# Optimization experiments

Hardware: AMD Instinct MI355X
Metric: run time of the kernel (lower is better)

Reference implementation:

```python
import jax, jax.numpy as jnp
import numpy as np

EPS = 1e-6
NEG_SLOPE = 0.2
B, C, E, F = 8, 2048, 256, 256


def setup_inputs() -> dict:
    key = jax.random.key(0)
    k1, k2, k3, k4, k5, k6 = jax.random.split(key, 6)
    X = jax.random.normal(k1, (B, C, E, 3), dtype=jnp.float32)
    J = jax.random.normal(k2, (B, C, E, 3), dtype=jnp.float32)
    A = jax.random.normal(k3, (F, E), dtype=jnp.float32)
    Bw = jax.random.normal(k4, (F, E), dtype=jnp.float32)
    Cw = jax.random.normal(k5, (F, E), dtype=jnp.float32)
    # VNLeakyReLU map_to_dir weight [F, F] (nn.Linear-style scale)
    W = jax.random.normal(k6, (F, F), dtype=jnp.float32) / jnp.sqrt(jnp.float32(F))
    return {"X": X, "J": J, "A": A, "Bw": Bw, "Cw": Cw, "W": W}


def _basis(J):
    # normalized direction [B,C,E,3]
    nJ = J / (jnp.linalg.norm(J, axis=-1, keepdims=True) + EPS)
    sub = nJ[..., :2]                                   # [B,C,E,2]
    Uz = -(sub * sub).sum(-1) / (nJ[..., 2] + EPS)      # [B,C,E]
    U = jnp.concatenate([sub, Uz[..., None]], axis=-1)  # [B,C,E,3]
    nU = U / (jnp.linalg.norm(U, axis=-1, keepdims=True) + EPS)
    nV = jnp.cross(nU, nJ)                              # [B,C,E,3]
    # rows of R are (U, V, J): R[..., i, j] matches torch reshape of cat
    return jnp.stack([nU, nV, nJ], axis=-2)             # [B,C,E,3,3]


def reference(X, J, A, Bw, Cw, W):
    R = _basis(J)                                        # [B,C,E,3,3]
    RT = jnp.swapaxes(R, -1, -2)                         # [B,C,E,3,3]
    # rtx[..., i] = RT[..., i, :] . X  (per torch get_rtx)
    rtx = jnp.einsum('bceij,bcej->bcei', RT, X)          # [B,C,E,3]

    def rrtx(i, r):
        # indexed_R = R[..., :, i]; broadcast-multiply by scalar field r
        return R[..., :, i] * r[..., None]               # [B,C,E,3]

    a = rrtx(0, rtx[..., 0]) + rrtx(1, rtx[..., 1])
    b = rrtx(1, rtx[..., 0]) - rrtx(0, rtx[..., 1])
    c = rrtx(2, rtx[..., 2])
    Y = (jnp.einsum('fe,bcei->bcfi', A, a)
         + jnp.einsum('fe,bcei->bcfi', Bw, b)
         + jnp.einsum('fe,bcei->bcfi', Cw, c))           # [B,C,F,3]

    x = jnp.transpose(Y, (0, 2, 3, 1))                   # [B,F,3,C]
    # VNLeakyReLU: direction d via linear over feature dim
    d = jnp.einsum('fg,bgic->bfic', W, x)                # [B,F,3,C]
    dot = (x * d).sum(axis=2, keepdims=True)             # [B,F,1,C]
    mask = (dot >= 0).astype(x.dtype)
    dns = (d * d).sum(axis=2, keepdims=True)
    x_out = (NEG_SLOPE * x
             + (1.0 - NEG_SLOPE) * (mask * x
                                    + (1.0 - mask) * (x - dot / (dns + EPS) * d)))
    return x_out
```

## Files before the change

### kernel.cpp

```cpp
#include <hip/hip_runtime.h>


constexpr float EPSf  = 1e-6f;
constexpr int Bdim = 8, Cdim = 2048, Edim = 256, Fdim = 256;
constexpr int NT  = 16;
constexpr int KC1 = 24;
constexpr int KC2 = 8;
constexpr int ZLD = 776;
constexpr int YLD = 264;
constexpr int M_ROWS = KC1 * 16 * 64;
constexpr int W_ROWS = KC2 * 16 * 64;

typedef __attribute__((ext_vector_type(8))) _Float16 half8;
typedef __attribute__((ext_vector_type(4))) _Float16 half4;
typedef __attribute__((ext_vector_type(4))) float    f32x4;

__device__ __forceinline__ void basis_abc(float Xx, float Xy, float Xz,
                                          float Jx, float Jy, float Jz,
                                          float* a, float* bb, float* cc)
{
    const float jn  = sqrtf(Jx*Jx + Jy*Jy + Jz*Jz) + EPSf;
    const float rj  = __builtin_amdgcn_rcpf(jn);
    const float nJz = Jz * rj;
    const float h   = (Jx*Jx + Jy*Jy) * (rj * rj);
    const float Uz  = -h * __builtin_amdgcn_rcpf(nJz + EPSf);
    const float un  = sqrtf(h + Uz*Uz) + EPSf;
    const float mx  = Uz * __builtin_amdgcn_rcpf(un);
    const float mz  = nJz;
    const float t   = mx*Xx + mz*Xz;
    a[0]  = Xx - mx*t;   a[1]  = Xy;            a[2]  = Xz - mz*t;
    bb[0] = mz*Xy;       bb[1] = mx*Xz - mz*Xx; bb[2] = -(mx*Xy);
    cc[0] = mx*t;        cc[1] = 0.f;           cc[2] = mz*t;
}

__global__ __launch_bounds__(256)
void prep_weights_f16(const float* __restrict__ Ap, const float* __restrict__ Bp,
                      const float* __restrict__ Cp, const float* __restrict__ Wp,
                      _Float16* __restrict__ ws)
{
    const int tid = blockIdx.x * 256 + threadIdx.x;
    const bool isW = tid >= M_ROWS;
    const int row = isW ? tid - M_ROWS : tid;
    const int l   = row & 63;
    const int ft  = (row >> 6) & 15;
    const int kc  = row >> 10;
    const int f   = ft * 16 + (l & 15);
    const int k0  = kc * 32 + ((l >> 4) << 3);

    const float* src;
    int e0;
    if (isW)            { src = Wp; e0 = k0; }
    else if (k0 < 256)  { src = Ap; e0 = k0; }
    else if (k0 < 512)  { src = Bp; e0 = k0 - 256; }
    else                { src = Cp; e0 = k0 - 512; }

    const float* p = src + f * 256 + e0;
    half8 v;
    #pragma unroll
    for (int j = 0; j < 8; ++j) v[j] = (_Float16)p[j];

    _Float16* dst = ws + (isW ? (size_t)M_ROWS * 8 : 0);
    *reinterpret_cast<half8*>(dst + (size_t)row * 8) = v;
}

__global__ __launch_bounds__(512, 4)
void fused_mfma_f16(const float* __restrict__ Xp, const float* __restrict__ Jp,
                    const _Float16* __restrict__ wsM, const _Float16* __restrict__ wsW,
                    float* __restrict__ outp)
{
    __shared__ __align__(16) _Float16 lds[48 * ZLD];

    const int t  = threadIdx.x;
    const int s0 = blockIdx.x * NT;
    const int b  = s0 >> 11;
    const int c0 = s0 & (Cdim - 1);

    {
        const int equad = t & 63;
        const int sq    = t >> 6;
        const int e0    = equad * 4;
        #pragma unroll
        for (int ss = 0; ss < 2; ++ss) {
            const int s = sq * 2 + ss;
            const long site = (long)(b * Cdim + c0 + s);
            const float4* X4 = reinterpret_cast<const float4*>(Xp) + site * 192 + equad * 3;
            const float4* J4 = reinterpret_cast<const float4*>(Jp) + site * 192 + equad * 3;
            const float4 xA = X4[0], xB = X4[1], xC = X4[2];
            const float4 jA = J4[0], jB = J4[1], jC = J4[2];
            const float xf[12] = {xA.x,xA.y,xA.z,xA.w, xB.x,xB.y,xB.z,xB.w, xC.x,xC.y,xC.z,xC.w};
            const float jf[12] = {jA.x,jA.y,jA.z,jA.w, jB.x,jB.y,jB.z,jB.w, jC.x,jC.y,jC.z,jC.w};

            half4 za[3], zb[3], zc[3];
            #pragma unroll
            for (int ee = 0; ee < 4; ++ee) {
                float a[3], bb[3], cc[3];
                basis_abc(xf[3*ee], xf[3*ee+1], xf[3*ee+2],
                          jf[3*ee], jf[3*ee+1], jf[3*ee+2], a, bb, cc);
                #pragma unroll
                for (int i = 0; i < 3; ++i) {
                    za[i][ee] = (_Float16)a[i];
                    zb[i][ee] = (_Float16)bb[i];
                    zc[i][ee] = (_Float16)cc[i];
                }
            }
            #pragma unroll
            for (int i = 0; i < 3; ++i) {
                _Float16* rowp = &lds[(i * NT + s) * ZLD];
                *reinterpret_cast<half4*>(rowp +       e0) = za[i];
                *reinterpret_cast<half4*>(rowp + 256 + e0) = zb[i];
                *reinterpret_cast<half4*>(rowp + 512 + e0) = zc[i];
            }
        }
    }
    __syncthreads();

    const int wid = t >> 6;
    const int l   = t & 63;
    const int lr  = l & 15;
    const int lk  = (l >> 4) * 8;

    f32x4 Yacc[2][3];
    #pragma unroll
    for (int q = 0; q < 2; ++q)
        #pragma unroll
        for (int nt = 0; nt < 3; ++nt)
            Yacc[q][nt] = f32x4{0.f, 0.f, 0.f, 0.f};

    const half8* Mf = reinterpret_cast<const half8*>(wsM);
    for (int kc = 0; kc < KC1; ++kc) {
        half8 af[2];
        #pragma unroll
        for (int q = 0; q < 2; ++q)
            af[q] = Mf[(kc * 16 + wid * 2 + q) * 64 + l];
        half8 zf[3];
        #pragma unroll
        for (int nt = 0; nt < 3; ++nt)
            zf[nt] = *reinterpret_cast<const half8*>(&lds[(nt * NT + lr) * ZLD + kc * 32 + lk]);
        #pragma unroll
        for (int q = 0; q < 2; ++q)
            #pragma unroll
            for (int nt = 0; nt < 3; ++nt)
                Yacc[q][nt] = __builtin_amdgcn_mfma_f32_16x16x32_f16(af[q], zf[nt], Yacc[q][nt], 0, 0, 0);
    }
    __syncthreads();

    #pragma unroll
    for (int q = 0; q < 2; ++q) {
        const int row = (wid * 2 + q) * 16 + (l >> 4) * 4;
        #pragma unroll
        for (int nt = 0; nt < 3; ++nt) {
            const int col = nt * NT + lr;
            half4 v = { (_Float16)Yacc[q][nt][0], (_Float16)Yacc[q][nt][1],
                        (_Float16)Yacc[q][nt][2], (_Float16)Yacc[q][nt][3] };
            *reinterpret_cast<half4*>(&lds[col * YLD + row]) = v;
        }
    }
    __syncthreads();

    f32x4 Dacc[2][3];
    #pragma unroll
    for (int q = 0; q < 2; ++q)
        #pragma unroll
        for (int nt = 0; nt < 3; ++nt)
            Dacc[q][nt] = f32x4{0.f, 0.f, 0.f, 0.f};

    const half8* Wf = reinterpret_cast<const half8*>(wsW);
    for (int kc = 0; kc < KC2; ++kc) {
        half8 af[2];
        #pragma unroll
        for (int q = 0; q < 2; ++q)
            af[q] = Wf[(kc * 16 + wid * 2 + q) * 64 + l];
        half8 yf[3];
        #pragma unroll
        for (int nt = 0; nt < 3; ++nt)
            yf[nt] = *reinterpret_cast<const half8*>(&lds[(nt * NT + lr) * YLD + kc * 32 + lk]);
        #pragma unroll
        for (int q = 0; q < 2; ++q)
            #pragma unroll
            for (int nt = 0; nt < 3; ++nt)
                Dacc[q][nt] = __builtin_amdgcn_mfma_f32_16x16x32_f16(af[q], yf[nt], Dacc[q][nt], 0, 0, 0);
    }

    #pragma unroll
    for (int q = 0; q < 2; ++q) {
        const int fbase = (wid * 2 + q) * 16 + (l >> 4) * 4;
        #pragma unroll
        for (int r = 0; r < 4; ++r) {
#pragma clang fp contract(off)
            const float x0 = Yacc[q][0][r], x1 = Yacc[q][1][r], x2 = Yacc[q][2][r];
            const float d0 = Dacc[q][0][r], d1 = Dacc[q][1][r], d2 = Dacc[q][2][r];
            const float dot = (x0*d0 + x1*d1) + x2*d2;
            const float dns = (d0*d0 + d1*d1) + d2*d2;
            const float sc  = dot / (dns + EPSf);
            const bool  pos = (dot >= 0.f);
            const int f = fbase + r;
            const long obase = ((long)(b * Fdim + f) * 3) * Cdim + c0 + lr;
            const float c0v = pos ? x0 : (x0 - sc*d0);
            const float c1v = pos ? x1 : (x1 - sc*d1);
            const float c2v = pos ? x2 : (x2 - sc*d2);
            outp[obase + 0 * Cdim] = 0.2f*x0 + 0.8f*c0v;
            outp[obase + 1 * Cdim] = 0.2f*x1 + 0.8f*c1v;
            outp[obase + 2 * Cdim] = 0.2f*x2 + 0.8f*c2v;
        }
    }
}

__device__ __forceinline__ float comp(const float4& v, int k) {
    return k == 0 ? v.x : k == 1 ? v.y : k == 2 ? v.z : v.w;
}

__global__ __launch_bounds__(256)
void fused_cl_lrelu_fp32(const float* __restrict__ Xp, const float* __restrict__ Jp,
                         const float* __restrict__ Ap, const float* __restrict__ Bp,
                         const float* __restrict__ Cp, const float* __restrict__ Wp,
                         float* __restrict__ outp)
{
    __shared__ float4 sabc[4 * Edim * 3];
    __shared__ float  ylds[4 * 3][Fdim];

    const int t   = threadIdx.x;
    const int s0  = blockIdx.x * 4;
    const int b   = s0 / Cdim;
    const int c0  = s0 % Cdim;

    #pragma unroll
    for (int r = 0; r < 4; ++r) {
        const int e  = t;
        const int idx = ((b * Cdim + c0 + r) * Edim + e) * 3;
        float a[3], bb[3], cc[3];
        basis_abc(Xp[idx], Xp[idx+1], Xp[idx+2], Jp[idx], Jp[idx+1], Jp[idx+2], a, bb, cc);
        const int base = (r * Edim + e) * 3;
        sabc[base + 0] = make_float4(a[0], a[1], a[2], bb[0]);
        sabc[base + 1] = make_float4(bb[1], bb[2], cc[0], cc[1]);
        sabc[base + 2] = make_float4(cc[2], 0.f, 0.f, 0.f);
    }
    __syncthreads();

    const int fl = t & 63;
    const int cg = t >> 6;
    float Y[4][3];
    #pragma unroll
    for (int q = 0; q < 4; ++q) Y[q][0] = Y[q][1] = Y[q][2] = 0.f;

    const float4* A4 = reinterpret_cast<const float4*>(Ap);
    const float4* B4 = reinterpret_cast<const float4*>(Bp);
    const float4* C4 = reinterpret_cast<const float4*>(Cp);
    for (int e4 = 0; e4 < Edim / 4; ++e4) {
        float4 wa[4], wb[4], wc[4];
        #pragma unroll
        for (int q = 0; q < 4; ++q) {
            const int f = q * 64 + fl;
            wa[q] = A4[f * (Edim/4) + e4];
            wb[q] = B4[f * (Edim/4) + e4];
            wc[q] = C4[f * (Edim/4) + e4];
        }
        #pragma unroll
        for (int k = 0; k < 4; ++k) {
            const int e = e4 * 4 + k;
            const float4 p0 = sabc[(cg * Edim + e) * 3 + 0];
            const float4 p1 = sabc[(cg * Edim + e) * 3 + 1];
            const float4 p2 = sabc[(cg * Edim + e) * 3 + 2];
            #pragma unroll
            for (int q = 0; q < 4; ++q) {
                const float Af = comp(wa[q], k), Bf = comp(wb[q], k), Cf = comp(wc[q], k);
                Y[q][0] += Af * p0.x + Bf * p0.w + Cf * p1.z;
                Y[q][1] += Af * p0.y + Bf * p1.x + Cf * p1.w;
                Y[q][2] += Af * p0.z + Bf * p1.y + Cf * p2.x;
            }
        }
    }
    #pragma unroll
    for (int q = 0; q < 4; ++q) {
        const int f = q * 64 + fl;
        ylds[cg * 3 + 0][f] = Y[q][0];
        ylds[cg * 3 + 1][f] = Y[q][1];
        ylds[cg * 3 + 2][f] = Y[q][2];
    }
    __syncthreads();

    float D[4][3];
    #pragma unroll
    for (int q = 0; q < 4; ++q) D[q][0] = D[q][1] = D[q][2] = 0.f;
    const float4* W4 = reinterpret_cast<const float4*>(Wp);
    for (int g4 = 0; g4 < Fdim / 4; ++g4) {
        float4 ww[4];
        #pragma unroll
        for (int q = 0; q < 4; ++q) ww[q] = W4[(q * 64 + fl) * (Fdim/4) + g4];
        const float4 y0 = *reinterpret_cast<const float4*>(&ylds[cg * 3 + 0][g4 * 4]);
        const float4 y1 = *reinterpret_cast<const float4*>(&ylds[cg * 3 + 1][g4 * 4]);
        const float4 y2 = *reinterpret_cast<const float4*>(&ylds[cg * 3 + 2][g4 * 4]);
        #pragma unroll
        for (int k = 0; k < 4; ++k) {
            #pragma unroll
            for (int q = 0; q < 4; ++q) {
                const float Wv = comp(ww[q], k);
                D[q][0] += Wv * comp(y0, k);
                D[q][1] += Wv * comp(y1, k);
                D[q][2] += Wv * comp(y2, k);
            }
        }
    }

    float* outl = reinterpret_cast<float*>(sabc);
    #pragma unroll
    for (int q = 0; q < 4; ++q) {
        const int f = q * 64 + fl;
        const float dot = (Y[q][0]*D[q][0] + Y[q][1]*D[q][1]) + Y[q][2]*D[q][2];
        const float dns = (D[q][0]*D[q][0] + D[q][1]*D[q][1]) + D[q][2]*D[q][2];
        const float s   = dot / (dns + EPSf);
        const bool  pos = (dot >= 0.f);
        #pragma unroll
        for (int i = 0; i < 3; ++i) {
            const float x = Y[q][i], d = D[q][i];
            outl[(f * 3 + i) * 4 + cg] = 0.2f*x + 0.8f*(pos ? x : x - s*d);
        }
    }
    __syncthreads();
    const float4* o4 = reinterpret_cast<const float4*>(outl);
    float4* O4 = reinterpret_cast<float4*>(outp);
    const int c4 = c0 >> 2;
    #pragma unroll
    for (int i = 0; i < 3; ++i)
        O4[((b * Fdim + t) * 3 + i) * (Cdim / 4) + c4] = o4[t * 3 + i];
}

extern "C" void kernel_launch(void* const* d_in, const int* in_sizes, int n_in,
                              void* d_out, int out_size, void* d_ws, size_t ws_size,
                              hipStream_t stream) {
    const float* X  = (const float*)d_in[0];
    const float* J  = (const float*)d_in[1];
    const float* A  = (const float*)d_in[2];
    const float* Bw = (const float*)d_in[3];
    const float* Cw = (const float*)d_in[4];
    const float* W  = (const float*)d_in[5];
    float* out = (float*)d_out;

    constexpr size_t WS_NEED = (size_t)(M_ROWS + W_ROWS) * 8 * sizeof(_Float16);
    if (ws_size >= WS_NEED) {
        _Float16* wsM = (_Float16*)d_ws;
        _Float16* wsW = wsM + (size_t)M_ROWS * 8;
        prep_weights_f16<<<(M_ROWS + W_ROWS) / 256, 256, 0, stream>>>(A, Bw, Cw, W, wsM);
        fused_mfma_f16<<<Bdim * Cdim / NT, 512, 0, stream>>>(X, J, wsM, wsW, out);
    } else {
        fused_cl_lrelu_fp32<<<Bdim * Cdim / 4, 256, 0, stream>>>(X, J, A, Bw, Cw, W, out);
    }
}
```

Measured before the change: 56.65 us.

## Fold W into combined weights to compute direction GEMM directly from Z

Precomputes W·[A|B|C] in a separate prep kernel and stores it as f16, so the fused kernel accumulates both Y and D in one pass over the rotated inputs. This removes the LDS staging of Y, two barriers and the second small GEMM. In exchange it roughly doubles the MFMA work and weight-fragment loads in the main loop, and adds a naive fp32 prep GEMM launch. Rounding behavior of D changes as well.

Result: slower. 93.69 us (+65.4%).

```diff
diff --git a/kernel.cpp b/kernel.cpp
--- a/kernel.cpp
+++ b/kernel.cpp
@@ -63,9 +63,52 @@
     *reinterpret_cast<half8*>(dst + (size_t)row * 8) = v;
 }
 
+__global__ __launch_bounds__(256)
+void prep_wm_f16(const float* __restrict__ Ap, const float* __restrict__ Bp,
+                 const float* __restrict__ Cp, const float* __restrict__ Wp,
+                 _Float16* __restrict__ wsWM)
+{
+    const int row = blockIdx.x * 256 + threadIdx.x;
+    const int l   = row & 63;
+    const int ft  = (row >> 6) & 15;
+    const int kc  = row >> 10;
+    const int f   = ft * 16 + (l & 15);
+    const int k0  = kc * 32 + ((l >> 4) << 3);
+
+    const float* src;
+    int e0;
+    if (k0 < 256)      { src = Ap; e0 = k0; }
+    else if (k0 < 512) { src = Bp; e0 = k0 - 256; }
+    else               { src = Cp; e0 = k0 - 512; }
+
+    const float4* S4 = reinterpret_cast<const float4*>(src);
+    const float*  Wr = Wp + f * 256;
+    const int e4 = e0 >> 2;
+
+    float acc[8];
+    #pragma unroll
+    for (int j = 0; j < 8; ++j) acc[j] = 0.f;
+
+    for (int g = 0; g < 256; g += 4) {
+        const float4 w4 = *reinterpret_cast<const float4*>(Wr + g);
+        #pragma unroll
+        for (int u = 0; u < 4; ++u) {
+            const float wv = (u == 0) ? w4.x : (u == 1) ? w4.y : (u == 2) ? w4.z : w4.w;
+            const float4 vA = S4[(g + u) * 64 + e4];
+            const float4 vB = S4[(g + u) * 64 + e4 + 1];
+            acc[0] += wv * vA.x; acc[1] += wv * vA.y; acc[2] += wv * vA.z; acc[3] += wv * vA.w;
+            acc[4] += wv * vB.x; acc[5] += wv * vB.y; acc[6] += wv * vB.z; acc[7] += wv * vB.w;
+        }
+    }
+    half8 v;
+    #pragma unroll
+    for (int j = 0; j < 8; ++j) v[j] = (_Float16)acc[j];
+    *reinterpret_cast<half8*>(wsWM + (size_t)row * 8) = v;
+}
+
 __global__ __launch_bounds__(512, 4)
-void fused_mfma_f16(const float* __restrict__ Xp, const float* __restrict__ Jp,
-                    const _Float16* __restrict__ wsM, const _Float16* __restrict__ wsW,
+void fused_fold_f16(const float* __restrict__ Xp, const float* __restrict__ Jp,
+                    const _Float16* __restrict__ wsM, const _Float16* __restrict__ wsWM,
                     float* __restrict__ outp)
 {
     __shared__ __align__(16) _Float16 lds[48 * ZLD];
@@ -119,19 +162,24 @@
     const int lr  = l & 15;
     const int lk  = (l >> 4) * 8;
 
-    f32x4 Yacc[2][3];
+    f32x4 Yacc[2][3], Dacc[2][3];
     #pragma unroll
     for (int q = 0; q < 2; ++q)
         #pragma unroll
-        for (int nt = 0; nt < 3; ++nt)
+        for (int nt = 0; nt < 3; ++nt) {
             Yacc[q][nt] = f32x4{0.f, 0.f, 0.f, 0.f};
+            Dacc[q][nt] = f32x4{0.f, 0.f, 0.f, 0.f};
+        }
 
     const half8* Mf = reinterpret_cast<const half8*>(wsM);
+    const half8* Gf = reinterpret_cast<const half8*>(wsWM);
     for (int kc = 0; kc < KC1; ++kc) {
-        half8 af[2];
-        #pragma unroll
-        for (int q = 0; q < 2; ++q)
+        half8 af[2], gf[2];
+        #pragma unroll
+        for (int q = 0; q < 2; ++q) {
             af[q] = Mf[(kc * 16 + wid * 2 + q) * 64 + l];
+            gf[q] = Gf[(kc * 16 + wid * 2 + q) * 64 + l];
+        }
         half8 zf[3];
         #pragma unroll
         for (int nt = 0; nt < 3; ++nt)
@@ -139,46 +187,10 @@
         #pragma unroll
         for (int q = 0; q < 2; ++q)
             #pragma unroll
-            for (int nt = 0; nt < 3; ++nt)
+            for (int nt = 0; nt < 3; ++nt) {
                 Yacc[q][nt] = __builtin_amdgcn_mfma_f32_16x16x32_f16(af[q], zf[nt], Yacc[q][nt], 0, 0, 0);
-    }
-    __syncthreads();
-
-    #pragma unroll
-    for (int q = 0; q < 2; ++q) {
-        const int row = (wid * 2 + q) * 16 + (l >> 4) * 4;
-        #pragma unroll
-        for (int nt = 0; nt < 3; ++nt) {
-            const int col = nt * NT + lr;
-            half4 v = { (_Float16)Yacc[q][nt][0], (_Float16)Yacc[q][nt][1],
-                        (_Float16)Yacc[q][nt][2], (_Float16)Yacc[q][nt][3] };
-            *reinterpret_cast<half4*>(&lds[col * YLD + row]) = v;
-        }
-    }
-    __syncthreads();
-
-    f32x4 Dacc[2][3];
-    #pragma unroll
-    for (int q = 0; q < 2; ++q)
-        #pragma unroll
-        for (int nt = 0; nt < 3; ++nt)
-            Dacc[q][nt] = f32x4{0.f, 0.f, 0.f, 0.f};
-
-    const half8* Wf = reinterpret_cast<const half8*>(wsW);
-    for (int kc = 0; kc < KC2; ++kc) {
-        half8 af[2];
-        #pragma unroll
-        for (int q = 0; q < 2; ++q)
-            af[q] = Wf[(kc * 16 + wid * 2 + q) * 64 + l];
-        half8 yf[3];
-        #pragma unroll
-        for (int nt = 0; nt < 3; ++nt)
-            yf[nt] = *reinterpret_cast<const half8*>(&lds[(nt * NT + lr) * YLD + kc * 32 + lk]);
-        #pragma unroll
-        for (int q = 0; q < 2; ++q)
-            #pragma unroll
-            for (int nt = 0; nt < 3; ++nt)
-                Dacc[q][nt] = __builtin_amdgcn_mfma_f32_16x16x32_f16(af[q], yf[nt], Dacc[q][nt], 0, 0, 0);
+                Dacc[q][nt] = __builtin_amdgcn_mfma_f32_16x16x32_f16(gf[q], zf[nt], Dacc[q][nt], 0, 0, 0);
+            }
     }
 
     #pragma unroll
@@ -205,6 +217,147 @@
     }
 }
 
+__global__ __launch_bounds__(512, 4)
+void fused_mfma_f16(const float* __restrict__ Xp, const float* __restrict__ Jp,
+                    const _Float16* __restrict__ wsM, const _Float16* __restrict__ wsW,
+                    float* __restrict__ outp)
+{
+    __shared__ __align__(16) _Float16 lds[48 * ZLD];
+
+    const int t  = threadIdx.x;
+    const int s0 = blockIdx.x * NT;
+    const int b  = s0 >> 11;
+    const int c0 = s0 & (Cdim - 1);
+
+    {
+        const int equad = t & 63;
+        const int sq    = t >> 6;
+        const int e0    = equad * 4;
+        #pragma unroll
+        for (int ss = 0; ss < 2; ++ss) {
+            const int s = sq * 2 + ss;
+            const long site = (long)(b * Cdim + c0 + s);
+            const float4* X4 = reinterpret_cast<const float4*>(Xp) + site * 192 + equad * 3;
+            const float4* J4 = reinterpret_cast<const float4*>(Jp) + site * 192 + equad * 3;
+            const float4 xA = X4[0], xB = X4[1], xC = X4[2];
+            const float4 jA = J4[0], jB = J4[1], jC = J4[2];
+            const float xf[12] = {xA.x,xA.y,xA.z,xA.w, xB.x,xB.y,xB.z,xB.w, xC.x,xC.y,xC.z,xC.w};
+            const float jf[12] = {jA.x,jA.y,jA.z,jA.w, jB.x,jB.y,jB.z,jB.w, jC.x,jC.y,jC.z,jC.w};
+            half4 za[3], zb[3], zc[3];
+            #pragma unroll
+            for (int ee = 0; ee < 4; ++ee) {
+                float a[3], bb[3], cc[3];
+                basis_abc(xf[3*ee], xf[3*ee+1], xf[3*ee+2],
+                          jf[3*ee], jf[3*ee+1], jf[3*ee+2], a, bb, cc);
+                #pragma unroll
+                for (int i = 0; i < 3; ++i) {
+                    za[i][ee] = (_Float16)a[i];
+                    zb[i][ee] = (_Float16)bb[i];
+                    zc[i][ee] = (_Float16)cc[i];
+                }
+            }
+            #pragma unroll
+            for (int i = 0; i < 3; ++i) {
+                _Float16* rowp = &lds[(i * NT + s) * ZLD];
+                *reinterpret_cast<half4*>(rowp +       e0) = za[i];
+                *reinterpret_cast<half4*>(rowp + 256 + e0) = zb[i];
+                *reinterpret_cast<half4*>(rowp + 512 + e0) = zc[i];
+            }
+        }
+    }
+    __syncthreads();
+
+    const int wid = t >> 6;
+    const int l   = t & 63;
+    const int lr  = l & 15;
+    const int lk  = (l >> 4) * 8;
+
+    f32x4 Yacc[2][3];
+    #pragma unroll
+    for (int q = 0; q < 2; ++q)
+        #pragma unroll
+        for (int nt = 0; nt < 3; ++nt)
+            Yacc[q][nt] = f32x4{0.f, 0.f, 0.f, 0.f};
+
+    const half8* Mf = reinterpret_cast<const half8*>(wsM);
+    for (int kc = 0; kc < KC1; ++kc) {
+        half8 af[2];
+        #pragma unroll
+        for (int q = 0; q < 2; ++q)
+            af[q] = Mf[(kc * 16 + wid * 2 + q) * 64 + l];
+        half8 zf[3];
+        #pragma unroll
+        for (int nt = 0; nt < 3; ++nt)
+            zf[nt] = *reinterpret_cast<const half8*>(&lds[(nt * NT + lr) * ZLD + kc * 32 + lk]);
+        #pragma unroll
+        for (int q = 0; q < 2; ++q)
+            #pragma unroll
+            for (int nt = 0; nt < 3; ++nt)
+                Yacc[q][nt] = __builtin_amdgcn_mfma_f32_16x16x32_f16(af[q], zf[nt], Yacc[q][nt], 0, 0, 0);
+    }
+    __syncthreads();
+
+    #pragma unroll
+    for (int q = 0; q < 2; ++q) {
+        const int row = (wid * 2 + q) * 16 + (l >> 4) * 4;
+        #pragma unroll
+        for (int nt = 0; nt < 3; ++nt) {
+            const int col = nt * NT + lr;
+            half4 v = { (_Float16)Yacc[q][nt][0], (_Float16)Yacc[q][nt][1],
+                        (_Float16)Yacc[q][nt][2], (_Float16)Yacc[q][nt][3] };
+            *reinterpret_cast<half4*>(&lds[col * YLD + row]) = v;
+        }
+    }
+    __syncthreads();
+
+    f32x4 Dacc[2][3];
+    #pragma unroll
+    for (int q = 0; q < 2; ++q)
+        #pragma unroll
+        for (int nt = 0; nt < 3; ++nt)
+            Dacc[q][nt] = f32x4{0.f, 0.f, 0.f, 0.f};
+
+    const half8* Wf = reinterpret_cast<const half8*>(wsW);
+    for (int kc = 0; kc < KC2; ++kc) {
+        half8 af[2];
+        #pragma unroll
+        for (int q = 0; q < 2; ++q)
+            af[q] = Wf[(kc * 16 + wid * 2 + q) * 64 + l];
+        half8 yf[3];
+        #pragma unroll
+        for (int nt = 0; nt < 3; ++nt)
+            yf[nt] = *reinterpret_cast<const half8*>(&lds[(nt * NT + lr) * YLD + kc * 32 + lk]);
+        #pragma unroll
+        for (int q = 0; q < 2; ++q)
+            #pragma unroll
+            for (int nt = 0; nt < 3; ++nt)
+                Dacc[q][nt] = __builtin_amdgcn_mfma_f32_16x16x32_f16(af[q], yf[nt], Dacc[q][nt], 0, 0, 0);
+    }
+
+    #pragma unroll
+    for (int q = 0; q < 2; ++q) {
+        const int fbase = (wid * 2 + q) * 16 + (l >> 4) * 4;
+        #pragma unroll
+        for (int r = 0; r < 4; ++r) {
+#pragma clang fp contract(off)
+            const float x0 = Yacc[q][0][r], x1 = Yacc[q][1][r], x2 = Yacc[q][2][r];
+            const float d0 = Dacc[q][0][r], d1 = Dacc[q][1][r], d2 = Dacc[q][2][r];
+            const float dot = (x0*d0 + x1*d1) + x2*d2;
+            const float dns = (d0*d0 + d1*d1) + d2*d2;
+            const float sc  = dot / (dns + EPSf);
+            const bool  pos = (dot >= 0.f);
+            const int f = fbase + r;
+            const long obase = ((long)(b * Fdim + f) * 3) * Cdim + c0 + lr;
+            const float c0v = pos ? x0 : (x0 - sc*d0);
+            const float c1v = pos ? x1 : (x1 - sc*d1);
+            const float c2v = pos ? x2 : (x2 - sc*d2);
+            outp[obase + 0 * Cdim] = 0.2f*x0 + 0.8f*c0v;
+            outp[obase + 1 * Cdim] = 0.2f*x1 + 0.8f*c1v;
+            outp[obase + 2 * Cdim] = 0.2f*x2 + 0.8f*c2v;
+        }
+    }
+}
+
 __device__ __forceinline__ float comp(const float4& v, int k) {
     return k == 0 ? v.x : k == 1 ? v.y : k == 2 ? v.z : v.w;
 }
@@ -335,10 +488,18 @@
     const float* W  = (const float*)d_in[5];
     float* out = (float*)d_out;
 
-    constexpr size_t WS_NEED = (size_t)(M_ROWS + W_ROWS) * 8 * sizeof(_Float16);
-    if (ws_size >= WS_NEED) {
-        _Float16* wsM = (_Float16*)d_ws;
-        _Float16* wsW = wsM + (size_t)M_ROWS * 8;
+    constexpr size_t NEED_BASE = (size_t)(M_ROWS + W_ROWS) * 8 * sizeof(_Float16);
+    constexpr size_t NEED_FOLD = NEED_BASE + (size_t)M_ROWS * 8 * sizeof(_Float16);
+
+    _Float16* wsM  = (_Float16*)d_ws;
+    _Float16* wsW  = wsM + (size_t)M_ROWS * 8;
+    _Float16* wsWM = wsM + (size_t)(M_ROWS + W_ROWS) * 8;
+
+    if (ws_size >= NEED_FOLD) {
+        prep_weights_f16<<<(M_ROWS + W_ROWS) / 256, 256, 0, stream>>>(A, Bw, Cw, W, wsM);
+        prep_wm_f16<<<M_ROWS / 256, 256, 0, stream>>>(A, Bw, Cw, W, wsWM);
+        fused_fold_f16<<<Bdim * Cdim / NT, 512, 0, stream>>>(X, J, wsM, wsWM, out);
+    } else if (ws_size >= NEED_BASE) {
         prep_weights_f16<<<(M_ROWS + W_ROWS) / 256, 256, 0, stream>>>(A, Bw, Cw, W, wsM);
         fused_mfma_f16<<<Bdim * Cdim / NT, 512, 0, stream>>>(X, J, wsM, wsW, out);
     } else {
```

## Store Z and Y tiles in LDS in MFMA fragment order and skip zero c-terms

Applied to the files above, without the earlier changes.

The LDS staging buffers for the per-site basis terms and the intermediate Y are rearranged so each lane reads its half8 MFMA operand as one contiguous, conflict-free vector indexed by lane id. This replaces the padded row-strided layout. The prologue now has each thread handle 8 consecutive e-values for one site, giving full half8 stores. For the last 8 k-chunks (the Cw term), the middle component of c is always zero, so its LDS write and MFMAs are skipped. Correctness depends on the new index math matching the 16x16x32 operand layout, and the wider per-thread prologue raises register pressure.

New measurement: 57.24 us, median of 2. About the same (+1.0%).

```diff
diff --git a/kernel.cpp b/kernel.cpp
--- a/kernel.cpp
+++ b/kernel.cpp
@@ -6,8 +6,6 @@
 constexpr int NT  = 16;
 constexpr int KC1 = 24;
 constexpr int KC2 = 8;
-constexpr int ZLD = 776;
-constexpr int YLD = 264;
 constexpr int M_ROWS = KC1 * 16 * 64;
 constexpr int W_ROWS = KC2 * 16 * 64;
 
@@ -68,7 +66,7 @@
                     const _Float16* __restrict__ wsM, const _Float16* __restrict__ wsW,
                     float* __restrict__ outp)
 {
-    __shared__ __align__(16) _Float16 lds[48 * ZLD];
+    __shared__ __align__(16) _Float16 lds[KC1 * 3 * 512];
 
     const int t  = threadIdx.x;
     const int s0 = blockIdx.x * NT;
@@ -76,40 +74,44 @@
     const int c0 = s0 & (Cdim - 1);
 
     {
-        const int equad = t & 63;
-        const int sq    = t >> 6;
-        const int e0    = equad * 4;
-        #pragma unroll
-        for (int ss = 0; ss < 2; ++ss) {
-            const int s = sq * 2 + ss;
-            const long site = (long)(b * Cdim + c0 + s);
-            const float4* X4 = reinterpret_cast<const float4*>(Xp) + site * 192 + equad * 3;
-            const float4* J4 = reinterpret_cast<const float4*>(Jp) + site * 192 + equad * 3;
-            const float4 xA = X4[0], xB = X4[1], xC = X4[2];
-            const float4 jA = J4[0], jB = J4[1], jC = J4[2];
-            const float xf[12] = {xA.x,xA.y,xA.z,xA.w, xB.x,xB.y,xB.z,xB.w, xC.x,xC.y,xC.z,xC.w};
-            const float jf[12] = {jA.x,jA.y,jA.z,jA.w, jB.x,jB.y,jB.z,jB.w, jC.x,jC.y,jC.z,jC.w};
-
-            half4 za[3], zb[3], zc[3];
-            #pragma unroll
-            for (int ee = 0; ee < 4; ++ee) {
-                float a[3], bb[3], cc[3];
-                basis_abc(xf[3*ee], xf[3*ee+1], xf[3*ee+2],
-                          jf[3*ee], jf[3*ee+1], jf[3*ee+2], a, bb, cc);
-                #pragma unroll
-                for (int i = 0; i < 3; ++i) {
-                    za[i][ee] = (_Float16)a[i];
-                    zb[i][ee] = (_Float16)bb[i];
-                    zc[i][ee] = (_Float16)cc[i];
-                }
+        const int s  = t & 15;
+        const int ep = t >> 4;
+        const long site = (long)(b * Cdim + c0 + s);
+        const float4* X4 = reinterpret_cast<const float4*>(Xp) + site * 192 + ep * 6;
+        const float4* J4 = reinterpret_cast<const float4*>(Jp) + site * 192 + ep * 6;
+
+        float xf[24], jf[24];
+        #pragma unroll
+        for (int u = 0; u < 6; ++u) {
+            const float4 xv = X4[u];
+            const float4 jv = J4[u];
+            xf[4*u+0] = xv.x; xf[4*u+1] = xv.y; xf[4*u+2] = xv.z; xf[4*u+3] = xv.w;
+            jf[4*u+0] = jv.x; jf[4*u+1] = jv.y; jf[4*u+2] = jv.z; jf[4*u+3] = jv.w;
+        }
+
+        half8 za8[3], zb8[3], zc8[3];
+        #pragma unroll
+        for (int pt = 0; pt < 8; ++pt) {
+            float a[3], bb[3], cc[3];
+            basis_abc(xf[3*pt], xf[3*pt+1], xf[3*pt+2],
+                      jf[3*pt], jf[3*pt+1], jf[3*pt+2], a, bb, cc);
+            #pragma unroll
+            for (int i = 0; i < 3; ++i) {
+                za8[i][pt] = (_Float16)a[i];
+                zb8[i][pt] = (_Float16)bb[i];
+                zc8[i][pt] = (_Float16)cc[i];
             }
-            #pragma unroll
-            for (int i = 0; i < 3; ++i) {
-                _Float16* rowp = &lds[(i * NT + s) * ZLD];
-                *reinterpret_cast<half4*>(rowp +       e0) = za[i];
-                *reinterpret_cast<half4*>(rowp + 256 + e0) = zb[i];
-                *reinterpret_cast<half4*>(rowp + 512 + e0) = zc[i];
-            }
+        }
+
+        half8* Zf = reinterpret_cast<half8*>(lds);
+        const int kcb  = ep >> 2;
+        const int slot = (ep & 3) * 16 + s;
+        #pragma unroll
+        for (int i = 0; i < 3; ++i) {
+            Zf[((kcb     ) * 3 + i) * 64 + slot] = za8[i];
+            Zf[((kcb +  8) * 3 + i) * 64 + slot] = zb8[i];
+            if (i != 1)
+                Zf[((kcb + 16) * 3 + i) * 64 + slot] = zc8[i];
         }
     }
     __syncthreads();
@@ -117,7 +119,7 @@
     const int wid = t >> 6;
     const int l   = t & 63;
     const int lr  = l & 15;
-    const int lk  = (l >> 4) * 8;
+    const int hi  = l >> 4;
 
     f32x4 Yacc[2][3];
     #pragma unroll
@@ -127,7 +129,9 @@
             Yacc[q][nt] = f32x4{0.f, 0.f, 0.f, 0.f};
 
     const half8* Mf = reinterpret_cast<const half8*>(wsM);
-    for (int kc = 0; kc < KC1; ++kc) {
+    const half8* Zf = reinterpret_cast<const half8*>(lds);
+
+    for (int kc = 0; kc < 16; ++kc) {
         half8 af[2];
         #pragma unroll
         for (int q = 0; q < 2; ++q)
@@ -135,24 +139,40 @@
         half8 zf[3];
         #pragma unroll
         for (int nt = 0; nt < 3; ++nt)
-            zf[nt] = *reinterpret_cast<const half8*>(&lds[(nt * NT + lr) * ZLD + kc * 32 + lk]);
+            zf[nt] = Zf[(kc * 3 + nt) * 64 + l];
         #pragma unroll
         for (int q = 0; q < 2; ++q)
             #pragma unroll
             for (int nt = 0; nt < 3; ++nt)
                 Yacc[q][nt] = __builtin_amdgcn_mfma_f32_16x16x32_f16(af[q], zf[nt], Yacc[q][nt], 0, 0, 0);
     }
+    for (int kc = 16; kc < KC1; ++kc) {
+        half8 af[2];
+        #pragma unroll
+        for (int q = 0; q < 2; ++q)
+            af[q] = Mf[(kc * 16 + wid * 2 + q) * 64 + l];
+        const half8 zf0 = Zf[(kc * 3 + 0) * 64 + l];
+        const half8 zf2 = Zf[(kc * 3 + 2) * 64 + l];
+        #pragma unroll
+        for (int q = 0; q < 2; ++q) {
+            Yacc[q][0] = __builtin_amdgcn_mfma_f32_16x16x32_f16(af[q], zf0, Yacc[q][0], 0, 0, 0);
+            Yacc[q][2] = __builtin_amdgcn_mfma_f32_16x16x32_f16(af[q], zf2, Yacc[q][2], 0, 0, 0);
+        }
+    }
     __syncthreads();
 
     #pragma unroll
     for (int q = 0; q < 2; ++q) {
-        const int row = (wid * 2 + q) * 16 + (l >> 4) * 4;
+        const int f0  = (wid * 2 + q) * 16 + hi * 4;
+        const int kc2 = f0 >> 5;
+        const int sub = (f0 >> 3) & 3;
+        const int j0  = f0 & 7;
         #pragma unroll
         for (int nt = 0; nt < 3; ++nt) {
-            const int col = nt * NT + lr;
             half4 v = { (_Float16)Yacc[q][nt][0], (_Float16)Yacc[q][nt][1],
                         (_Float16)Yacc[q][nt][2], (_Float16)Yacc[q][nt][3] };
-            *reinterpret_cast<half4*>(&lds[col * YLD + row]) = v;
+            const int idx = ((kc2 * 3 + nt) * 64 + sub * 16 + lr) * 8 + j0;
+            *reinterpret_cast<half4*>(&lds[idx]) = v;
         }
     }
     __syncthreads();
@@ -165,25 +185,26 @@
             Dacc[q][nt] = f32x4{0.f, 0.f, 0.f, 0.f};
 
     const half8* Wf = reinterpret_cast<const half8*>(wsW);
+    const half8* Yf = reinterpret_cast<const half8*>(lds);
     for (int kc = 0; kc < KC2; ++kc) {
-        half8 af[2];
-        #pragma unroll
-        for (int q = 0; q < 2; ++q)
-            af[q] = Wf[(kc * 16 + wid * 2 + q) * 64 + l];
+        half8 wf[2];
+        #pragma unroll
+        for (int q = 0; q < 2; ++q)
+            wf[q] = Wf[(kc * 16 + wid * 2 + q) * 64 + l];
         half8 yf[3];
         #pragma unroll
         for (int nt = 0; nt < 3; ++nt)
-            yf[nt] = *reinterpret_cast<const half8*>(&lds[(nt * NT + lr) * YLD + kc * 32 + lk]);
+            yf[nt] = Yf[(kc * 3 + nt) * 64 + l];
         #pragma unroll
         for (int q = 0; q < 2; ++q)
             #pragma unroll
             for (int nt = 0; nt < 3; ++nt)
-                Dacc[q][nt] = __builtin_amdgcn_mfma_f32_16x16x32_f16(af[q], yf[nt], Dacc[q][nt], 0, 0, 0);
+                Dacc[q][nt] = __builtin_amdgcn_mfma_f32_16x16x32_f16(wf[q], yf[nt], Dacc[q][nt], 0, 0, 0);
     }
 
     #pragma unroll
     for (int q = 0; q < 2; ++q) {
-        const int fbase = (wid * 2 + q) * 16 + (l >> 4) * 4;
+        const int fbase = (wid * 2 + q) * 16 + hi * 4;
         #pragma unroll
         for (int r = 0; r < 4; ++r) {
 #pragma clang fp contract(off)
```
